# Kernel tuning notes

Measured on AMD Instinct MI355X. Metric: run time of the kernel, lower is better.

## Reference

```python
import jax, jax.numpy as jnp
import numpy as np

B, T, H, W, C = 1, 16, 56, 56, 256
NH = 8
WS = (8, 7, 7)
SS = (4, 3, 3)
HID = 4 * C
N = WS[0] * WS[1] * WS[2]  # 392 tokens per window


def _rel_index(ws):
    wt, wh, ww = ws
    coords = np.stack(np.meshgrid(np.arange(wt), np.arange(wh), np.arange(ww), indexing='ij'))
    cf = coords.reshape(3, -1)
    rel = (cf[:, :, None] - cf[:, None, :]).transpose(1, 2, 0)
    rel[..., 0] += wt - 1
    rel[..., 1] += wh - 1
    rel[..., 2] += ww - 1
    rel[..., 0] *= (2 * wh - 1) * (2 * ww - 1)
    rel[..., 1] *= 2 * ww - 1
    return rel.sum(-1)  # (N, N) int


def _win_part_np(x, ws):
    b, t, h, w, c = x.shape
    x = x.reshape(b, t // ws[0], ws[0], h // ws[1], ws[1], w // ws[2], ws[2], c)
    return x.transpose(0, 1, 3, 5, 2, 4, 6, 7).reshape(-1, ws[0] * ws[1] * ws[2], c)


def _attn_mask(t, h, w, ws, ss):
    # static numpy construction of the shifted-window mask (nW, N, N)
    img = np.zeros((1, t, h, w, 1), dtype=np.float32)
    cnt = 0
    for d in (slice(-ws[0]), slice(-ws[0], -ss[0]), slice(-ss[0], None)):
        for hh in (slice(-ws[1]), slice(-ws[1], -ss[1]), slice(-ss[1], None)):
            for ww_ in (slice(-ws[2]), slice(-ws[2], -ss[2]), slice(-ss[2], None)):
                img[:, d, hh, ww_, :] = cnt
                cnt += 1
    mw = _win_part_np(img, ws).squeeze(-1)  # (nW, N)
    diff = mw[:, None, :] - mw[:, :, None]
    return np.where(diff != 0, np.float32(-100.0), np.float32(0.0))


_RPI = jnp.asarray(_rel_index(WS).reshape(-1))
_MASK = jnp.asarray(_attn_mask(T, H, W, WS, SS))  # (nW, N, N)


def _ln(x, g, b, eps=1e-5):
    mu = x.mean(-1, keepdims=True)
    var = ((x - mu) ** 2).mean(-1, keepdims=True)
    return (x - mu) * jax.lax.rsqrt(var + eps) * g + b


def _win_part(x, ws):
    b, t, h, w, c = x.shape
    x = x.reshape(b, t // ws[0], ws[0], h // ws[1], ws[1], w // ws[2], ws[2], c)
    return x.transpose(0, 1, 3, 5, 2, 4, 6, 7).reshape(-1, ws[0] * ws[1] * ws[2], c)


def _win_rev(win, ws, t, h, w):
    b = win.shape[0] // (t * h * w // (ws[0] * ws[1] * ws[2]))
    x = win.reshape(b, t // ws[0], h // ws[1], w // ws[2], ws[0], ws[1], ws[2], -1)
    return x.transpose(0, 1, 4, 2, 5, 3, 6, 7).reshape(b, t, h, w, -1)


def setup_inputs() -> dict:
    key = jax.random.key(0)
    ks = jax.random.split(key, 16)
    n_bias = (2 * WS[0] - 1) * (2 * WS[1] - 1) * (2 * WS[2] - 1)
    return {
        'x': jax.random.normal(ks[0], (B, T, H, W, C), jnp.float32),
        'norm1_g': jnp.ones((C,), jnp.float32),
        'norm1_b': jnp.zeros((C,), jnp.float32),
        'qkv_w': 0.02 * jax.random.normal(ks[1], (3 * C, C), jnp.float32),
        'qkv_b': jnp.zeros((3 * C,), jnp.float32),
        'rpb_table': 0.02 * jax.random.normal(ks[2], (n_bias, NH), jnp.float32),
        'proj_w': 0.02 * jax.random.normal(ks[3], (C, C), jnp.float32),
        'proj_b': jnp.zeros((C,), jnp.float32),
        'norm2_g': jnp.ones((C,), jnp.float32),
        'norm2_b': jnp.zeros((C,), jnp.float32),
        'fc1_w': 0.02 * jax.random.normal(ks[4], (HID, C), jnp.float32),
        'fc1_b': jnp.zeros((HID,), jnp.float32),
        'fc2_w': 0.02 * jax.random.normal(ks[5], (C, HID), jnp.float32),
        'fc2_b': jnp.zeros((C,), jnp.float32),
    }


def reference(x, norm1_g, norm1_b, qkv_w, qkv_b, rpb_table, proj_w, proj_b,
              norm2_g, norm2_b, fc1_w, fc1_b, fc2_w, fc2_b):
    hd = C // NH
    scale = hd ** -0.5
    shortcut = x
    h1 = _ln(x, norm1_g, norm1_b)
    # cyclic shift
    h1 = jnp.roll(h1, (-SS[0], -SS[1], -SS[2]), axis=(1, 2, 3))
    xw = _win_part(h1, WS)  # (B_, N, C)
    B_ = xw.shape[0]
    qkv = xw @ qkv_w.T + qkv_b  # (B_, N, 3C)
    qkv = qkv.reshape(B_, N, 3, NH, hd).transpose(2, 0, 3, 1, 4)
    q, k, v = qkv[0], qkv[1], qkv[2]  # (B_, NH, N, hd)
    attn = jnp.einsum('bhnd,bhmd->bhnm', q * scale, k)
    bias = rpb_table[_RPI].reshape(N, N, NH).transpose(2, 0, 1)  # (NH, N, N)
    attn = attn + bias[None]
    nW = _MASK.shape[0]
    attn = attn.reshape(B_ // nW, nW, NH, N, N) + _MASK[None, :, None]
    attn = jax.nn.softmax(attn, axis=-1).reshape(B_, NH, N, N)
    out = jnp.einsum('bhnm,bhmd->bhnd', attn, v).transpose(0, 2, 1, 3).reshape(B_, N, C)
    out = out @ proj_w.T + proj_b
    out = _win_rev(out, WS, T, H, W)
    out = jnp.roll(out, (SS[0], SS[1], SS[2]), axis=(1, 2, 3))
    x = shortcut + out
    # MLP with residual
    h2 = _ln(x, norm2_g, norm2_b)
    h2 = jax.nn.gelu(h2 @ fc1_w.T + fc1_b, approximate=False)
    return x + (h2 @ fc2_w.T + fc2_b)
```

## Files before the change

kernel.cpp:

```cpp
#include <hip/hip_runtime.h>
#include <hip/hip_bf16.h>
#include <cmath>

typedef unsigned short u16;
typedef unsigned int u32;

using bf16x8 = __attribute__((ext_vector_type(8))) short;
using f32x4  = __attribute__((ext_vector_type(4))) float;

__device__ __forceinline__ float b2f(u16 u) {
  union { u32 i; float f; } x; x.i = ((u32)u) << 16; return x.f;
}
__device__ __forceinline__ u16 f2b(float f) {
  union { float f; u32 i; } x; x.f = f;
  u32 r = x.i + 0x7fffu + ((x.i >> 16) & 1u);
  return (u16)(r >> 16);
}
__device__ __forceinline__ u32 cvtpk(float lo, float hi) {
  u32 r;
  asm("v_cvt_pk_bf16_f32 %0, %1, %2" : "=v"(r) : "v"(lo), "v"(hi));
  return r;
}
__device__ __forceinline__ float vexp2(float x) {
  float r;
  asm("v_exp_f32 %0, %1" : "=v"(r) : "v"(x));
  return r;
}
__device__ __forceinline__ void gload_lds16(const u16* g, u16* l) {
  __builtin_amdgcn_global_load_lds(
      (const __attribute__((address_space(1))) unsigned int*)g,
      (__attribute__((address_space(3))) unsigned int*)l, 16, 0, 0);
}

__global__ __launch_bounds__(256) void castw(const float* __restrict__ qkvw,
                                             const float* __restrict__ projw,
                                             const float* __restrict__ fc1w,
                                             const float* __restrict__ fc2w,
                                             u16* __restrict__ o) {
  int i = blockIdx.x * 256 + threadIdx.x;
  const float* src;
  int off;
  if (i < 196608)      { src = qkvw;  off = 0; }
  else if (i < 262144) { src = projw; off = 196608; }
  else if (i < 524288) { src = fc1w;  off = 262144; }
  else                 { src = fc2w;  off = 524288; }
  o[i] = f2b(src[i - off]);
}

__global__ __launch_bounds__(256) void bias_k(const float* __restrict__ rpb,
                                              u16* __restrict__ biasB,
                                              float* __restrict__ rowmax) {
  const int b = blockIdx.x;
  const int sl = b / 25, qt = b - sl * 25;
  const int head = sl & 7, cls = sl >> 3;
  const int tb = (cls >> 2) & 1, hb = (cls >> 1) & 1, wb = cls & 1;
  const int tid = threadIdx.x;
  const int lm = tid >> 4, kl = tid & 15;
  int q = qt * 16 + lm; if (q > 391) q = 391;
  const int ti = q / 49, rem = q - ti * 49, hi = rem / 7, wi = rem - hi * 7;
  const int cq = ti * 169 + hi * 13 + wi;
  const int rtq = tb ? (ti < 4 ? 1 : 2) : 0;
  const int rhq = hb ? (hi < 4 ? 1 : 2) : 0;
  const int rwq = wb ? (wi < 4 ? 1 : 2) : 0;
  const int labq = rtq * 9 + rhq * 3 + rwq;
  float mx = -3e38f;
  u16* ob = biasB + (size_t)b * 6400 + tid;
  for (int t = 0; t < 25; t++) {
    int k = t * 16 + kl;
    float v;
    if (k < 392) {
      int tk = k / 49, rk = k - tk * 49, hk = rk / 7, wk = rk - hk * 7;
      int ck = tk * 169 + hk * 13 + wk;
      float bv = rpb[(cq - ck + 1267) * 8 + head];
      int rt = tb ? (tk < 4 ? 1 : 2) : 0;
      int rh = hb ? (hk < 4 ? 1 : 2) : 0;
      int rw = wb ? (wk < 4 ? 1 : 2) : 0;
      if (rt * 9 + rh * 3 + rw != labq) bv -= 100.f;
      v = bv * 1.4426950408889634f;
      mx = fmaxf(mx, v);
    } else {
      v = -2081.f;
    }
    ob[t * 256] = f2b(v);
  }
  mx = fmaxf(mx, __shfl_xor(mx, 1, 64));
  mx = fmaxf(mx, __shfl_xor(mx, 2, 64));
  mx = fmaxf(mx, __shfl_xor(mx, 4, 64));
  mx = fmaxf(mx, __shfl_xor(mx, 8, 64));
  if (kl == 0) rowmax[sl * 392 + q] = mx;
}

__global__ __launch_bounds__(256) void ln_k(const float* __restrict__ src,
                                            const float* __restrict__ g,
                                            const float* __restrict__ b,
                                            u16* __restrict__ dst, int shifted) {
  const int wid = threadIdx.x >> 6, lane = threadIdx.x & 63;
  const int row = blockIdx.x * 4 + wid;
  int srow;
  if (shifted) {
    int widx = row / 392, n = row - widx * 392;
    int wt = widx >> 6, wh = (widx >> 3) & 7, ww = widx & 7;
    int ti = n / 49, rem = n - ti * 49, hi = rem / 7, wi = rem - hi * 7;
    int t = (wt * 8 + ti + 4) & 15;
    int h = wh * 7 + hi + 3; if (h >= 56) h -= 56;
    int w = ww * 7 + wi + 3; if (w >= 56) w -= 56;
    srow = (t * 56 + h) * 56 + w;
  } else {
    srow = row;
  }
  float4 v = *(const float4*)(src + (size_t)srow * 256 + lane * 4);
  float s = v.x + v.y + v.z + v.w;
  float sq = v.x * v.x + v.y * v.y + v.z * v.z + v.w * v.w;
  for (int o = 1; o < 64; o <<= 1) {
    s += __shfl_xor(s, o, 64);
    sq += __shfl_xor(sq, o, 64);
  }
  float mu = s * (1.0f / 256.0f);
  float rstd = rsqrtf(sq * (1.0f / 256.0f) - mu * mu + 1e-5f);
  float4 gg = *(const float4*)(g + lane * 4);
  float4 bb = *(const float4*)(b + lane * 4);
  ushort4 ov;
  ov.x = f2b((v.x - mu) * rstd * gg.x + bb.x);
  ov.y = f2b((v.y - mu) * rstd * gg.y + bb.y);
  ov.z = f2b((v.z - mu) * rstd * gg.z + bb.z);
  ov.w = f2b((v.w - mu) * rstd * gg.w + bb.w);
  *(ushort4*)(dst + (size_t)row * 256 + lane * 4) = ov;
}

template <int EPI>
__global__ __launch_bounds__(512) void gemm_k(const u16* __restrict__ A,
                                              const u16* __restrict__ Bw,
                                              int K, int tilesN,
                                              const float* __restrict__ bias,
                                              u16* __restrict__ outb,
                                              float* __restrict__ outf,
                                              const float* __restrict__ res,
                                              float qscale) {
  __shared__ __align__(16) u16 As[2][256 * 32];
  __shared__ __align__(16) u16 Bs[2][128 * 32];
  const int tid = threadIdx.x;
  const int swzb = ((int)blockIdx.x & 7) * ((int)gridDim.x >> 3) +
                   ((int)blockIdx.x >> 3);
  const int tm = swzb / tilesN, tn = swzb - tm * tilesN;
  const int wid = tid >> 6, lane = tid & 63;
  const int wm = wid >> 1, wn = wid & 1;
  const int lm = lane & 15, lk = lane >> 4;
  f32x4 acc[4][4] = {};
  const u16* Ap = A + (size_t)tm * 256 * K;
  const u16* Bp = Bw + (size_t)tn * 128 * K;

  const int sA0 = wid * 128;
  const int sB0 = wid * 64;
  const int nt = K >> 5;

#define STAGE(bufi, kk)                                                       \
  {                                                                           \
    int S = sA0 + lane, r = S >> 2, cs = S & 3;                               \
    gload_lds16(Ap + (size_t)r * K + (kk) + ((cs ^ ((r >> 1) & 3)) << 3),     \
                &As[bufi][sA0 * 8]);                                          \
    S = sA0 + 64 + lane; r = S >> 2; cs = S & 3;                              \
    gload_lds16(Ap + (size_t)r * K + (kk) + ((cs ^ ((r >> 1) & 3)) << 3),     \
                &As[bufi][(sA0 + 64) * 8]);                                   \
    S = sB0 + lane; r = S >> 2; cs = S & 3;                                   \
    gload_lds16(Bp + (size_t)r * K + (kk) + ((cs ^ ((r >> 1) & 3)) << 3),     \
                &Bs[bufi][sB0 * 8]);                                          \
  }

  STAGE(0, 0);
  for (int t = 0; t < nt; t++) {
    const int cur = t & 1;
    if (t + 1 < nt) {
      STAGE(cur ^ 1, (t + 1) << 5);
      asm volatile("s_waitcnt vmcnt(3)" ::: "memory");
    } else {
      asm volatile("s_waitcnt vmcnt(0)" ::: "memory");
    }
    asm volatile("s_barrier" ::: "memory");
    __builtin_amdgcn_sched_barrier(0);
    bf16x8 af[4], bfr[4];
#pragma unroll
    for (int f = 0; f < 4; f++) {
      int ra = wm * 64 + f * 16 + lm;
      int rb = wn * 64 + f * 16 + lm;
      af[f] = *(const bf16x8*)((const char*)&As[cur][0] + ra * 64 +
                               ((lk ^ ((ra >> 1) & 3)) << 4));
      bfr[f] = *(const bf16x8*)((const char*)&Bs[cur][0] + rb * 64 +
                                ((lk ^ ((rb >> 1) & 3)) << 4));
    }
#pragma unroll
    for (int fm = 0; fm < 4; fm++)
#pragma unroll
      for (int fn = 0; fn < 4; fn++)
        acc[fm][fn] = __builtin_amdgcn_mfma_f32_16x16x32_bf16(
            af[fm], bfr[fn], acc[fm][fn], 0, 0, 0);
    asm volatile("s_barrier" ::: "memory");
  }
#undef STAGE

  const int rbase = tm * 256 + wm * 64, cbase = tn * 128 + wn * 64;
#pragma unroll
  for (int fm = 0; fm < 4; fm++) {
#pragma unroll
    for (int fn = 0; fn < 4; fn++) {
      const int col = cbase + fn * 16 + lm;
#pragma unroll
      for (int r = 0; r < 4; r++) {
        const int row = rbase + fm * 16 + lk * 4 + r;
        float v = acc[fm][fn][r] + bias[col];
        if (EPI == 0) {
          int s = col >> 8, rem = col & 255, head = rem >> 5, d = rem & 31;
          int widx = row / 392, n = row - widx * 392;
          size_t o;
          if (s == 2) {
            o = 25690112u + (((size_t)(widx * 8 + head)) * 32 + d) * 400 + n;
          } else {
            if (s == 0) v *= qscale;
            o = (size_t)s * 12845056u +
                (((size_t)(widx * 8 + head)) * 392 + n) * 32 + d;
          }
          outb[o] = f2b(v);
        } else if (EPI == 1) {
          int widx = row / 392, n = row - widx * 392;
          int wt = widx >> 6, wh = (widx >> 3) & 7, ww = widx & 7;
          int ti = n / 49, rem2 = n - ti * 49, hi = rem2 / 7, wi = rem2 - hi * 7;
          int t = (wt * 8 + ti + 4) & 15;
          int h = wh * 7 + hi + 3; if (h >= 56) h -= 56;
          int w = ww * 7 + wi + 3; if (w >= 56) w -= 56;
          size_t dr = ((size_t)(t * 56 + h)) * 56 + w;
          outf[dr * 256 + col] = res[dr * 256 + col] + v;
        } else if (EPI == 2) {
          float gv = 0.5f * v * (1.0f + erff(v * 0.70710678f));
          outb[(size_t)row * 1024 + col] = f2b(gv);
        } else {
          outf[(size_t)row * 256 + col] = res[(size_t)row * 256 + col] + v;
        }
      }
    }
  }
}

__global__ __launch_bounds__(256) void attn_k(const u16* __restrict__ qg,
                                              const u16* __restrict__ kg,
                                              const u16* __restrict__ vTg,
                                              const u16* __restrict__ biasB,
                                              u16* __restrict__ attno) {
  __shared__ __align__(16) char lds[58432];
  const int bid = blockIdx.x;
  const int widx = bid >> 3;
  const int tid = threadIdx.x;
  const size_t base = (size_t)bid * 12544;
  const int tb = (widx >> 6) & 1;
  const int hb = (((widx >> 3) & 7) == 7) ? 1 : 0;
  const int wb = ((widx & 7) == 7) ? 1 : 0;
  const int sl = (tb * 4 + hb * 2 + wb) * 8 + (bid & 7);
  const int VOFF = 25088;
  const int POFF = 50240;

#pragma unroll
  for (int i = 0; i < 6; i++) {
    int s = i * 256 + tid, r = s >> 2, cs = s & 3;
    gload_lds16(kg + base + r * 32 + ((cs ^ ((r >> 1) & 3)) << 3),
                (u16*)(lds + (size_t)(i * 256 + (tid & ~63)) * 16));
  }
  if (tid < 32) {
    int s = 1536 + tid, r = s >> 2, cs = s & 3;
    gload_lds16(kg + base + r * 32 + ((cs ^ ((r >> 1) & 3)) << 3),
                (u16*)(lds + (size_t)1536 * 16));
  }
  {
    const u16* vsrc = vTg + (size_t)bid * 12800;
    for (int idx = tid; idx < 3136; idx += 256) {
      int d = idx / 98, c4 = idx - d * 98;
      *(ushort4*)(lds + VOFF + d * 784 + c4 * 8) =
          *(const ushort4*)(vsrc + d * 400 + c4 * 4);
    }
    if (tid < 16) ((u32*)(lds + VOFF + 25088))[tid] = 0u;
  }
  __syncthreads();

  const int w = tid >> 6, lane = tid & 63;
  const int g = lane >> 4, lm = lane & 15;
  const int kswz = ((lm >> 1) & 3);
  char* PqW = lds + POFF + w * 2048 + lm * 128;
  const int swz = (lm & 7) << 4;

  for (int qt = w; qt < 25; qt += 4) {
    const int q = qt * 16 + lm;
    const int qr = q < 391 ? q : 391;
    bf16x8 qf = *(const bf16x8*)(qg + base + (size_t)qr * 32 + g * 8);
    const u16* bp = biasB + ((size_t)(sl * 25 + qt) * 25) * 256 + lm * 16 + 4 * g;
    f32x4 st[25];
#pragma unroll
    for (int t = 0; t < 25; t++) {
      ushort4 bb = *(const ushort4*)(bp + t * 256);
      f32x4 bacc = {b2f(bb.x), b2f(bb.y), b2f(bb.z), b2f(bb.w)};
      int kr = (t < 24) ? (16 * t + lm) : (384 + (lm & 7));
      bf16x8 kf = *(const bf16x8*)(lds + kr * 64 + ((g ^ kswz) << 4));
      st[t] = __builtin_amdgcn_mfma_f32_16x16x32_bf16(kf, qf, bacc, 0, 0, 0);
    }
    float m = -3e38f;
#pragma unroll
    for (int t = 0; t < 25; t++)
      m = fmaxf(m, fmaxf(fmaxf(st[t][0], st[t][1]), fmaxf(st[t][2], st[t][3])));
    m = fmaxf(m, __shfl_xor(m, 16, 64));
    m = fmaxf(m, __shfl_xor(m, 32, 64));

    float sum = 0.f;
    f32x4 oa0 = {0.f, 0.f, 0.f, 0.f}, oa1 = {0.f, 0.f, 0.f, 0.f};
#pragma unroll
    for (int c = 0; c < 13; c++) {
      const int p64 = (c & 1) << 6;
      {
        int t = 2 * c;
        float e0 = vexp2(st[t][0] - m), e1 = vexp2(st[t][1] - m);
        float e2 = vexp2(st[t][2] - m), e3 = vexp2(st[t][3] - m);
        sum += (e0 + e1) + (e2 + e3);
        uint2 pp;
        pp.x = cvtpk(e0, e1);
        pp.y = cvtpk(e2, e3);
        *(uint2*)(PqW + ((p64 + 8 * g) ^ swz)) = pp;
      }
      {
        uint2 pp;
        if (c < 12) {
          int t = 2 * c + 1;
          float e0 = vexp2(st[t][0] - m), e1 = vexp2(st[t][1] - m);
          float e2 = vexp2(st[t][2] - m), e3 = vexp2(st[t][3] - m);
          sum += (e0 + e1) + (e2 + e3);
          pp.x = cvtpk(e0, e1);
          pp.y = cvtpk(e2, e3);
        } else {
          pp.x = 0u; pp.y = 0u;
        }
        *(uint2*)(PqW + ((p64 + 32 + 8 * g) ^ swz)) = pp;
      }
      bf16x8 pf = *(const bf16x8*)(PqW + ((p64 + 16 * g) ^ swz));
      const char* vrow = lds + VOFF + 64 * c + 16 * g;
      bf16x8 v0 = *(const bf16x8*)(vrow + lm * 784);
      bf16x8 v1 = *(const bf16x8*)(vrow + (16 + lm) * 784);
      oa0 = __builtin_amdgcn_mfma_f32_16x16x32_bf16(pf, v0, oa0, 0, 0, 0);
      oa1 = __builtin_amdgcn_mfma_f32_16x16x32_bf16(pf, v1, oa1, 0, 0, 0);
    }
    sum += __shfl_xor(sum, 16, 64);
    sum += __shfl_xor(sum, 32, 64);
    const float inv = 1.f / sum;
#pragma unroll
    for (int r = 0; r < 4; r++) {
      int qq = qt * 16 + 4 * g + r;
      if (qq < 392) {
        u16* op = attno + ((size_t)(widx * 392 + qq)) * 256 + (bid & 7) * 32;
        op[lm] = f2b(oa0[r] * inv);
        op[16 + lm] = f2b(oa1[r] * inv);
      }
    }
  }
}

extern "C" void kernel_launch(void* const* d_in, const int* in_sizes, int n_in,
                              void* d_out, int out_size, void* d_ws,
                              size_t ws_size, hipStream_t stream) {
  const float* x     = (const float*)d_in[0];
  const float* n1g   = (const float*)d_in[1];
  const float* n1b   = (const float*)d_in[2];
  const float* qkvw  = (const float*)d_in[3];
  const float* qkvb  = (const float*)d_in[4];
  const float* rpb   = (const float*)d_in[5];
  const float* projw = (const float*)d_in[6];
  const float* projb = (const float*)d_in[7];
  const float* n2g   = (const float*)d_in[8];
  const float* n2b   = (const float*)d_in[9];
  const float* fc1w  = (const float*)d_in[10];
  const float* fc1b  = (const float*)d_in[11];
  const float* fc2w  = (const float*)d_in[12];
  const float* fc2b  = (const float*)d_in[13];

  const size_t NEED = 130547712;
  if (ws_size < NEED) return;

  char* ws = (char*)d_ws;
  u16* xw      = (u16*)(ws + 0LL);
  u16* qb      = (u16*)(ws + 25690112LL);
  u16* attno   = (u16*)(ws + 0LL);
  u16* hid     = (u16*)(ws + 0LL);
  u16* biasB   = (u16*)(ws + 103284736LL);
  float* rmx   = (float*)(ws + 123764736LL);
  u16* h2      = (u16*)(ws + 103284736LL);
  u16* wq      = (u16*)(ws + 128974848LL);
  u16* wp      = (u16*)(ws + 129368064LL);
  u16* w1      = (u16*)(ws + 129499136LL);
  u16* w2      = (u16*)(ws + 130023424LL);
  float* xres  = (float*)d_out;

  castw<<<3072, 256, 0, stream>>>(qkvw, projw, fc1w, fc2w, wq);
  bias_k<<<1600, 256, 0, stream>>>(rpb, biasB, rmx);

  ln_k<<<12544, 256, 0, stream>>>(x, n1g, n1b, xw, 1);
  gemm_k<0><<<196 * 6, 512, 0, stream>>>(
      xw, wq, 256, 6, qkvb, qb, nullptr, nullptr,
      0.17677669529663687f * 1.4426950408889634f);
  attn_k<<<1024, 256, 0, stream>>>(qb, qb + 12845056, qb + 2 * 12845056, biasB,
                                   attno);
  gemm_k<1><<<196 * 2, 512, 0, stream>>>(attno, wp, 256, 2, projb, nullptr,
                                         xres, x, 0.f);
  ln_k<<<12544, 256, 0, stream>>>(xres, n2g, n2b, h2, 0);
  gemm_k<2><<<196 * 8, 512, 0, stream>>>(h2, w1, 256, 8, fc1b, hid, nullptr,
                                         nullptr, 0.f);
  gemm_k<3><<<196 * 2, 512, 0, stream>>>(hid, w2, 1024, 2, fc2b, nullptr,
                                         (float*)d_out, xres, 0.f);
}
```

Baseline: 325.8 us.

## Merge setup kernels into one launch and read V directly from global

Folds the weight cast, bias/mask table build and first shifted LayerNorm into a single pre_k launch with block-range dispatch, and drops the unused row-max output. The attention kernel no longer stages transposed V into LDS; it reads V fragments straight from global memory, cutting LDS from about 58KB to 33KB. This removes launch overhead and the V staging copy, and may raise occupancy, but each V fragment is now fetched per MFMA step from global or cache instead of LDS.

```diff
diff --git a/kernel.cpp b/kernel.cpp
--- a/kernel.cpp
+++ b/kernel.cpp
@@ -32,83 +32,91 @@
       (__attribute__((address_space(3))) unsigned int*)l, 16, 0, 0);
 }
 
-__global__ __launch_bounds__(256) void castw(const float* __restrict__ qkvw,
-                                             const float* __restrict__ projw,
-                                             const float* __restrict__ fc1w,
-                                             const float* __restrict__ fc2w,
-                                             u16* __restrict__ o) {
-  int i = blockIdx.x * 256 + threadIdx.x;
-  const float* src;
-  int off;
-  if (i < 196608)      { src = qkvw;  off = 0; }
-  else if (i < 262144) { src = projw; off = 196608; }
-  else if (i < 524288) { src = fc1w;  off = 262144; }
-  else                 { src = fc2w;  off = 524288; }
-  o[i] = f2b(src[i - off]);
-}
-
-__global__ __launch_bounds__(256) void bias_k(const float* __restrict__ rpb,
-                                              u16* __restrict__ biasB,
-                                              float* __restrict__ rowmax) {
-  const int b = blockIdx.x;
-  const int sl = b / 25, qt = b - sl * 25;
-  const int head = sl & 7, cls = sl >> 3;
-  const int tb = (cls >> 2) & 1, hb = (cls >> 1) & 1, wb = cls & 1;
+__global__ __launch_bounds__(256) void pre_k(
+    const float* __restrict__ x, const float* __restrict__ n1g,
+    const float* __restrict__ n1b, const float* __restrict__ qkvw,
+    const float* __restrict__ projw, const float* __restrict__ fc1w,
+    const float* __restrict__ fc2w, const float* __restrict__ rpb,
+    u16* __restrict__ xw, u16* __restrict__ wts, u16* __restrict__ biasB) {
+  const int blk = blockIdx.x;
   const int tid = threadIdx.x;
-  const int lm = tid >> 4, kl = tid & 15;
-  int q = qt * 16 + lm; if (q > 391) q = 391;
-  const int ti = q / 49, rem = q - ti * 49, hi = rem / 7, wi = rem - hi * 7;
-  const int cq = ti * 169 + hi * 13 + wi;
-  const int rtq = tb ? (ti < 4 ? 1 : 2) : 0;
-  const int rhq = hb ? (hi < 4 ? 1 : 2) : 0;
-  const int rwq = wb ? (wi < 4 ? 1 : 2) : 0;
-  const int labq = rtq * 9 + rhq * 3 + rwq;
-  float mx = -3e38f;
-  u16* ob = biasB + (size_t)b * 6400 + tid;
-  for (int t = 0; t < 25; t++) {
-    int k = t * 16 + kl;
-    float v;
-    if (k < 392) {
-      int tk = k / 49, rk = k - tk * 49, hk = rk / 7, wk = rk - hk * 7;
-      int ck = tk * 169 + hk * 13 + wk;
-      float bv = rpb[(cq - ck + 1267) * 8 + head];
-      int rt = tb ? (tk < 4 ? 1 : 2) : 0;
-      int rh = hb ? (hk < 4 ? 1 : 2) : 0;
-      int rw = wb ? (wk < 4 ? 1 : 2) : 0;
-      if (rt * 9 + rh * 3 + rw != labq) bv -= 100.f;
-      v = bv * 1.4426950408889634f;
-      mx = fmaxf(mx, v);
-    } else {
-      v = -2081.f;
-    }
-    ob[t * 256] = f2b(v);
-  }
-  mx = fmaxf(mx, __shfl_xor(mx, 1, 64));
-  mx = fmaxf(mx, __shfl_xor(mx, 2, 64));
-  mx = fmaxf(mx, __shfl_xor(mx, 4, 64));
-  mx = fmaxf(mx, __shfl_xor(mx, 8, 64));
-  if (kl == 0) rowmax[sl * 392 + q] = mx;
-}
-
-__global__ __launch_bounds__(256) void ln_k(const float* __restrict__ src,
-                                            const float* __restrict__ g,
-                                            const float* __restrict__ b,
-                                            u16* __restrict__ dst, int shifted) {
-  const int wid = threadIdx.x >> 6, lane = threadIdx.x & 63;
-  const int row = blockIdx.x * 4 + wid;
-  int srow;
-  if (shifted) {
+  if (blk < 12544) {
+    const int wid = tid >> 6, lane = tid & 63;
+    const int row = blk * 4 + wid;
     int widx = row / 392, n = row - widx * 392;
     int wt = widx >> 6, wh = (widx >> 3) & 7, ww = widx & 7;
     int ti = n / 49, rem = n - ti * 49, hi = rem / 7, wi = rem - hi * 7;
     int t = (wt * 8 + ti + 4) & 15;
     int h = wh * 7 + hi + 3; if (h >= 56) h -= 56;
     int w = ww * 7 + wi + 3; if (w >= 56) w -= 56;
-    srow = (t * 56 + h) * 56 + w;
+    int srow = (t * 56 + h) * 56 + w;
+    float4 v = *(const float4*)(x + (size_t)srow * 256 + lane * 4);
+    float s = v.x + v.y + v.z + v.w;
+    float sq = v.x * v.x + v.y * v.y + v.z * v.z + v.w * v.w;
+    for (int o = 1; o < 64; o <<= 1) {
+      s += __shfl_xor(s, o, 64);
+      sq += __shfl_xor(sq, o, 64);
+    }
+    float mu = s * (1.0f / 256.0f);
+    float rstd = rsqrtf(sq * (1.0f / 256.0f) - mu * mu + 1e-5f);
+    float4 gg = *(const float4*)(n1g + lane * 4);
+    float4 bb = *(const float4*)(n1b + lane * 4);
+    ushort4 ov;
+    ov.x = f2b((v.x - mu) * rstd * gg.x + bb.x);
+    ov.y = f2b((v.y - mu) * rstd * gg.y + bb.y);
+    ov.z = f2b((v.z - mu) * rstd * gg.z + bb.z);
+    ov.w = f2b((v.w - mu) * rstd * gg.w + bb.w);
+    *(ushort4*)(xw + (size_t)row * 256 + lane * 4) = ov;
+  } else if (blk < 14144) {
+    const int b = blk - 12544;
+    const int sl = b / 25, qt = b - sl * 25;
+    const int head = sl & 7, cls = sl >> 3;
+    const int tb = (cls >> 2) & 1, hb = (cls >> 1) & 1, wb = cls & 1;
+    const int lm = tid >> 4, kl = tid & 15;
+    int q = qt * 16 + lm; if (q > 391) q = 391;
+    const int ti = q / 49, rem = q - ti * 49, hi = rem / 7, wi = rem - hi * 7;
+    const int cq = ti * 169 + hi * 13 + wi;
+    const int rtq = tb ? (ti < 4 ? 1 : 2) : 0;
+    const int rhq = hb ? (hi < 4 ? 1 : 2) : 0;
+    const int rwq = wb ? (wi < 4 ? 1 : 2) : 0;
+    const int labq = rtq * 9 + rhq * 3 + rwq;
+    u16* ob = biasB + (size_t)b * 6400 + tid;
+    for (int t = 0; t < 25; t++) {
+      int k = t * 16 + kl;
+      float v;
+      if (k < 392) {
+        int tk = k / 49, rk = k - tk * 49, hk = rk / 7, wk = rk - hk * 7;
+        int ck = tk * 169 + hk * 13 + wk;
+        float bv = rpb[(cq - ck + 1267) * 8 + head];
+        int rt = tb ? (tk < 4 ? 1 : 2) : 0;
+        int rh = hb ? (hk < 4 ? 1 : 2) : 0;
+        int rw = wb ? (wk < 4 ? 1 : 2) : 0;
+        if (rt * 9 + rh * 3 + rw != labq) bv -= 100.f;
+        v = bv * 1.4426950408889634f;
+      } else {
+        v = -2081.f;
+      }
+      ob[t * 256] = f2b(v);
+    }
   } else {
-    srow = row;
-  }
-  float4 v = *(const float4*)(src + (size_t)srow * 256 + lane * 4);
+    int i = (blk - 14144) * 256 + tid;
+    const float* src;
+    int off;
+    if (i < 196608)      { src = qkvw;  off = 0; }
+    else if (i < 262144) { src = projw; off = 196608; }
+    else if (i < 524288) { src = fc1w;  off = 262144; }
+    else                 { src = fc2w;  off = 524288; }
+    wts[i] = f2b(src[i - off]);
+  }
+}
+
+__global__ __launch_bounds__(256) void ln_k(const float* __restrict__ src,
+                                            const float* __restrict__ g,
+                                            const float* __restrict__ b,
+                                            u16* __restrict__ dst) {
+  const int wid = threadIdx.x >> 6, lane = threadIdx.x & 63;
+  const int row = blockIdx.x * 4 + wid;
+  float4 v = *(const float4*)(src + (size_t)row * 256 + lane * 4);
   float s = v.x + v.y + v.z + v.w;
   float sq = v.x * v.x + v.y * v.y + v.z * v.z + v.w * v.w;
   for (int o = 1; o < 64; o <<= 1) {
@@ -244,7 +252,7 @@
                                               const u16* __restrict__ vTg,
                                               const u16* __restrict__ biasB,
                                               u16* __restrict__ attno) {
-  __shared__ __align__(16) char lds[58432];
+  __shared__ __align__(16) char lds[33280];
   const int bid = blockIdx.x;
   const int widx = bid >> 3;
   const int tid = threadIdx.x;
@@ -253,8 +261,7 @@
   const int hb = (((widx >> 3) & 7) == 7) ? 1 : 0;
   const int wb = ((widx & 7) == 7) ? 1 : 0;
   const int sl = (tb * 4 + hb * 2 + wb) * 8 + (bid & 7);
-  const int VOFF = 25088;
-  const int POFF = 50240;
+  const int POFF = 25088;
 
 #pragma unroll
   for (int i = 0; i < 6; i++) {
@@ -266,15 +273,6 @@
     int s = 1536 + tid, r = s >> 2, cs = s & 3;
     gload_lds16(kg + base + r * 32 + ((cs ^ ((r >> 1) & 3)) << 3),
                 (u16*)(lds + (size_t)1536 * 16));
-  }
-  {
-    const u16* vsrc = vTg + (size_t)bid * 12800;
-    for (int idx = tid; idx < 3136; idx += 256) {
-      int d = idx / 98, c4 = idx - d * 98;
-      *(ushort4*)(lds + VOFF + d * 784 + c4 * 8) =
-          *(const ushort4*)(vsrc + d * 400 + c4 * 4);
-    }
-    if (tid < 16) ((u32*)(lds + VOFF + 25088))[tid] = 0u;
   }
   __syncthreads();
 
@@ -283,6 +281,7 @@
   const int kswz = ((lm >> 1) & 3);
   char* PqW = lds + POFF + w * 2048 + lm * 128;
   const int swz = (lm & 7) << 4;
+  const u16* vg_b = vTg + (size_t)bid * 12800;
 
   for (int qt = w; qt < 25; qt += 4) {
     const int q = qt * 16 + lm;
@@ -335,9 +334,9 @@
         *(uint2*)(PqW + ((p64 + 32 + 8 * g) ^ swz)) = pp;
       }
       bf16x8 pf = *(const bf16x8*)(PqW + ((p64 + 16 * g) ^ swz));
-      const char* vrow = lds + VOFF + 64 * c + 16 * g;
-      bf16x8 v0 = *(const bf16x8*)(vrow + lm * 784);
-      bf16x8 v1 = *(const bf16x8*)(vrow + (16 + lm) * 784);
+      const u16* vp = vg_b + lm * 400 + 32 * c + 8 * g;
+      bf16x8 v0 = *(const bf16x8*)vp;
+      bf16x8 v1 = *(const bf16x8*)(vp + 6400);
       oa0 = __builtin_amdgcn_mfma_f32_16x16x32_bf16(pf, v0, oa0, 0, 0, 0);
       oa1 = __builtin_amdgcn_mfma_f32_16x16x32_bf16(pf, v1, oa1, 0, 0, 0);
     }
@@ -383,7 +382,6 @@
   u16* attno   = (u16*)(ws + 0LL);
   u16* hid     = (u16*)(ws + 0LL);
   u16* biasB   = (u16*)(ws + 103284736LL);
-  float* rmx   = (float*)(ws + 123764736LL);
   u16* h2      = (u16*)(ws + 103284736LL);
   u16* wq      = (u16*)(ws + 128974848LL);
   u16* wp      = (u16*)(ws + 129368064LL);
@@ -391,10 +389,8 @@
   u16* w2      = (u16*)(ws + 130023424LL);
   float* xres  = (float*)d_out;
 
-  castw<<<3072, 256, 0, stream>>>(qkvw, projw, fc1w, fc2w, wq);
-  bias_k<<<1600, 256, 0, stream>>>(rpb, biasB, rmx);
-
-  ln_k<<<12544, 256, 0, stream>>>(x, n1g, n1b, xw, 1);
+  pre_k<<<17216, 256, 0, stream>>>(x, n1g, n1b, qkvw, projw, fc1w, fc2w, rpb,
+                                   xw, wq, biasB);
   gemm_k<0><<<196 * 6, 512, 0, stream>>>(
       xw, wq, 256, 6, qkvb, qb, nullptr, nullptr,
       0.17677669529663687f * 1.4426950408889634f);
@@ -402,7 +398,7 @@
                                    attno);
   gemm_k<1><<<196 * 2, 512, 0, stream>>>(attno, wp, 256, 2, projb, nullptr,
                                          xres, x, 0.f);
-  ln_k<<<12544, 256, 0, stream>>>(xres, n2g, n2b, h2, 0);
+  ln_k<<<12544, 256, 0, stream>>>(xres, n2g, n2b, h2);
   gemm_k<2><<<196 * 8, 512, 0, stream>>>(h2, w1, 256, 8, fc1b, hid, nullptr,
                                          nullptr, 0.f);
   gemm_k<3><<<196 * 2, 512, 0, stream>>>(hid, w2, 1024, 2, fc2b, nullptr,
```

After: 349.5 us. +7.3%, slower.
